# Performance work log

Measured on AMD Instinct MI355X. Metric: run time of the kernel, lower is better.

## Reference

```python
import jax, jax.numpy as jnp
import numpy as np

N_NODES = 50000
N_EDGES = 640000
IN_F, HID, OUT = 128, 128, 64
EPS = 1e-5


def _glorot(key, shape):
    fan_in, fan_out = shape
    lim = jnp.sqrt(6.0 / (fan_in + fan_out))
    return jax.random.uniform(key, shape, jnp.float32, -lim, lim)


def setup_inputs() -> dict:
    key = jax.random.key(0)
    ks = jax.random.split(key, 16)
    inp = {
        "x": jax.random.normal(ks[0], (N_NODES, IN_F), jnp.float32),
        "src": jax.random.randint(ks[1], (N_EDGES,), 0, N_NODES, jnp.int32),
        "dst": jax.random.randint(ks[2], (N_EDGES,), 0, N_NODES, jnp.int32),
        # layer 0: in -> hid
        "Ws0": _glorot(ks[3], (IN_F, HID)),
        "Wn0": _glorot(ks[4], (IN_F, HID)),
        "b0": jnp.zeros((HID,), jnp.float32),
        # layer 1: hid -> hid
        "Ws1": _glorot(ks[5], (HID, HID)),
        "Wn1": _glorot(ks[6], (HID, HID)),
        "b1": jnp.zeros((HID,), jnp.float32),
        # layer 2: hid -> out
        "Ws2": _glorot(ks[7], (HID, OUT)),
        "Wn2": _glorot(ks[8], (HID, OUT)),
        "b2": jnp.zeros((OUT,), jnp.float32),
        # batchnorm params for the two hidden layers
        "g0": jnp.ones((HID,), jnp.float32),
        "beta0": jnp.zeros((HID,), jnp.float32),
        "g1": jnp.ones((HID,), jnp.float32),
        "beta1": jnp.zeros((HID,), jnp.float32),
    }
    return inp


def _sage_conv(h, src, dst, Ws, Wn, b):
    # mean aggregation over in-neighbors (DGL SAGEConv 'mean')
    ones = jnp.ones_like(dst, dtype=h.dtype)
    deg = jax.ops.segment_sum(ones, dst, num_segments=N_NODES)
    agg = jax.ops.segment_sum(h[src], dst, num_segments=N_NODES)
    agg = agg / jnp.maximum(deg, 1.0)[:, None]
    return h @ Ws + agg @ Wn + b


def _batchnorm(h, gamma, beta):
    mu = jnp.mean(h, axis=0)
    var = jnp.mean(jnp.square(h - mu), axis=0)  # biased, like torch BN
    return (h - mu) * jax.lax.rsqrt(var + EPS) * gamma + beta


def reference(x, src, dst, Ws0, Wn0, b0, Ws1, Wn1, b1, Ws2, Wn2, b2,
              g0, beta0, g1, beta1):
    h = _sage_conv(x, src, dst, Ws0, Wn0, b0)
    h = jax.nn.relu(_batchnorm(h, g0, beta0))  # dropout = identity (eval)
    h = _sage_conv(h, src, dst, Ws1, Wn1, b1)
    h = jax.nn.relu(_batchnorm(h, g1, beta1))
    h = _sage_conv(h, src, dst, Ws2, Wn2, b2)
    return h
```

## Files before the change

### kernel.cpp

```cpp
#include <hip/hip_runtime.h>

#define N_NODES 50000
#define N_EDGES 640000
#define EPS 1e-5f
#define NBLK_SCAN 196

typedef __attribute__((ext_vector_type(8))) short short8;
typedef __attribute__((ext_vector_type(4))) float f32x4;

__device__ inline unsigned short f2bf(float f) {
    unsigned u = __float_as_uint(f);
    u += 0x7fffu + ((u >> 16) & 1u);
    return (unsigned short)(u >> 16);
}
__device__ inline float bf2f(unsigned short b) {
    return __uint_as_float(((unsigned)b) << 16);
}
__device__ inline void storev(short* p, float v) { *(unsigned short*)p = f2bf(v); }
__device__ inline void storev(float* p, float v) { *p = v; }

__global__ void hist_kernel(const int* __restrict__ dst, int* __restrict__ counts,
                            int* __restrict__ erank) {
    int i = blockIdx.x * 256 + threadIdx.x;
    if (i >= N_EDGES / 8) return;
    int4 a = ((const int4*)dst)[2 * i];
    int4 b = ((const int4*)dst)[2 * i + 1];
    int4 ra, rb;
    ra.x = atomicAdd(&counts[a.x], 1);
    ra.y = atomicAdd(&counts[a.y], 1);
    ra.z = atomicAdd(&counts[a.z], 1);
    ra.w = atomicAdd(&counts[a.w], 1);
    rb.x = atomicAdd(&counts[b.x], 1);
    rb.y = atomicAdd(&counts[b.y], 1);
    rb.z = atomicAdd(&counts[b.z], 1);
    rb.w = atomicAdd(&counts[b.w], 1);
    ((int4*)erank)[2 * i]     = ra;
    ((int4*)erank)[2 * i + 1] = rb;
}

__global__ void scan1_kernel(const int* __restrict__ counts, int* __restrict__ incl,
                             int* __restrict__ bsums) {
    __shared__ int tmp[256];
    int t = threadIdx.x;
    int i = blockIdx.x * 256 + t;
    tmp[t] = (i < N_NODES) ? counts[i] : 0;
    __syncthreads();
    for (int off = 1; off < 256; off <<= 1) {
        int add = (t >= off) ? tmp[t - off] : 0;
        __syncthreads();
        tmp[t] += add;
        __syncthreads();
    }
    if (i < N_NODES) incl[i] = tmp[t];
    if (t == 255) bsums[blockIdx.x] = tmp[255];
}

__global__ void scan2_kernel(const int* __restrict__ bsums, int* __restrict__ boff) {
    __shared__ int tmp[256];
    int t = threadIdx.x;
    tmp[t] = (t < NBLK_SCAN) ? bsums[t] : 0;
    __syncthreads();
    for (int off = 1; off < 256; off <<= 1) {
        int add = (t >= off) ? tmp[t - off] : 0;
        __syncthreads();
        tmp[t] += add;
        __syncthreads();
    }
    if (t < NBLK_SCAN) boff[t] = (t == 0) ? 0 : tmp[t - 1];
}

__global__ void scan3_kernel(const int* __restrict__ counts, const int* __restrict__ incl,
                             const int* __restrict__ boff, int* __restrict__ rowptr,
                             float* __restrict__ rdeg) {
    int i = blockIdx.x * 256 + threadIdx.x;
    if (i >= N_NODES) return;
    int c = counts[i];
    int inc = incl[i] + boff[blockIdx.x];
    rowptr[i] = inc - c;
    rdeg[i] = 1.0f / fmaxf((float)c, 1.0f);
    if (i == N_NODES - 1) rowptr[N_NODES] = inc;
}

__global__ void fill_kernel(const int* __restrict__ src, const int* __restrict__ dst,
                            const int* __restrict__ erank, const int* __restrict__ rowptr,
                            int* __restrict__ esrc) {
    int i = blockIdx.x * 256 + threadIdx.x;
    if (i >= N_EDGES / 8) return;
    int4 da = ((const int4*)dst)[2 * i];
    int4 db = ((const int4*)dst)[2 * i + 1];
    int4 sa = ((const int4*)src)[2 * i];
    int4 sb = ((const int4*)src)[2 * i + 1];
    int4 ra = ((const int4*)erank)[2 * i];
    int4 rb = ((const int4*)erank)[2 * i + 1];
    esrc[rowptr[da.x] + ra.x] = sa.x;
    esrc[rowptr[da.y] + ra.y] = sa.y;
    esrc[rowptr[da.z] + ra.z] = sa.z;
    esrc[rowptr[da.w] + ra.w] = sa.w;
    esrc[rowptr[db.x] + rb.x] = sb.x;
    esrc[rowptr[db.y] + rb.y] = sb.y;
    esrc[rowptr[db.z] + rb.z] = sb.z;
    esrc[rowptr[db.w] + rb.w] = sb.w;
}

__global__ void xcvt_kernel(const float* __restrict__ in, short* __restrict__ outp,
                            int* __restrict__ counts, float* __restrict__ stats) {
    int bi = blockIdx.x, t = threadIdx.x;
    if (bi == 0 && t < 128) {
        float4 z = make_float4(0.f, 0.f, 0.f, 0.f);
        ((float4*)stats)[t] = z;
    }
    if (bi >= 1 && bi <= NBLK_SCAN) {
        int idx = (bi - 1) * 256 + t;
        if (idx < N_NODES) counts[idx] = 0;
    }
    int i = bi * 256 + t;
    if (i >= N_NODES * 16) return;
    const float4* p = (const float4*)in + 2 * (size_t)i;
    float4 a = p[0], b = p[1];
    short8 v;
    v[0] = (short)f2bf(a.x); v[1] = (short)f2bf(a.y);
    v[2] = (short)f2bf(a.z); v[3] = (short)f2bf(a.w);
    v[4] = (short)f2bf(b.x); v[5] = (short)f2bf(b.y);
    v[6] = (short)f2bf(b.z); v[7] = (short)f2bf(b.w);
    *((short8*)outp + i) = v;
}

__global__ void pack_all(const float* __restrict__ W0, const float* __restrict__ W1,
                         const float* __restrict__ W2, const float* __restrict__ W3,
                         const float* __restrict__ W4, const float* __restrict__ W5,
                         short* __restrict__ P0, short* __restrict__ P1,
                         short* __restrict__ P2, short* __restrict__ P3,
                         short* __restrict__ P4, short* __restrict__ P5) {
    int b = blockIdx.x;
    const float* W; short* P; int NC; int base;
    if      (b < 8)  { W = W0; P = P0; NC = 128; base = 0;  }
    else if (b < 16) { W = W1; P = P1; NC = 128; base = 8;  }
    else if (b < 24) { W = W2; P = P2; NC = 128; base = 16; }
    else if (b < 32) { W = W3; P = P3; NC = 128; base = 24; }
    else if (b < 36) { W = W4; P = P4; NC = 64;  base = 32; }
    else             { W = W5; P = P5; NC = 64;  base = 36; }
    int idx = (b - base) * 256 + threadIdx.x;
    int total = 4 * (NC / 16) * 64;
    if (idx >= total) return;
    int lane = idx & 63;
    int cbks = idx >> 6;
    int cb = cbks % (NC / 16);
    int ks = cbks / (NC / 16);
    int col = cb * 16 + (lane & 15);
    int k0 = ks * 32 + ((lane >> 4) << 3);
    short8 v;
    #pragma unroll
    for (int j = 0; j < 8; ++j) v[j] = (short)f2bf(W[(size_t)(k0 + j) * NC + col]);
    *((short8*)P + idx) = v;
}

template<bool BN>
__global__ void gather_k(const short* __restrict__ h, const int* __restrict__ rowptr,
                         const int* __restrict__ esrc, const float* __restrict__ rdeg,
                         const float* __restrict__ sums, const float* __restrict__ sqs,
                         const float* __restrict__ g, const float* __restrict__ beta,
                         short* __restrict__ agg) {
    int node = blockIdx.x * 4 + (threadIdx.x >> 6);
    int lane = threadIdx.x & 63;
    if (node >= N_NODES) return;
    int beg = rowptr[node], end = rowptr[node + 1];
    float s0 = 0.f, s1 = 0.f, b0 = 0.f, b1 = 0.f;
    if (BN) {
        const float invN = 1.0f / N_NODES;
        float2 sm = *(const float2*)(sums + lane * 2);
        float2 sq = *(const float2*)(sqs + lane * 2);
        float2 gg = *(const float2*)(g + lane * 2);
        float2 bb = *(const float2*)(beta + lane * 2);
        float m0 = sm.x * invN, m1 = sm.y * invN;
        float v0 = sq.x * invN - m0 * m0, v1 = sq.y * invN - m1 * m1;
        s0 = rsqrtf(v0 + EPS) * gg.x;
        s1 = rsqrtf(v1 + EPS) * gg.y;
        b0 = bb.x - m0 * s0;
        b1 = bb.y - m1 * s1;
    }
    float ax = 0.f, ay = 0.f;
    while (beg < end) {
        int cnt = min(end - beg, 64);
        int mi = esrc[beg + min(lane, cnt - 1)];
        for (int j = 0; j < cnt; j += 16) {
            int lim = cnt - j; if (lim > 16) lim = 16;
            unsigned v[16];
            #pragma unroll
            for (int u = 0; u < 16; ++u) {
                int s = __shfl(mi, j + (u < lim ? u : lim - 1));
                v[u] = *(const unsigned*)(h + (size_t)s * 128 + lane * 2);
            }
            #pragma unroll
            for (int u = 0; u < 16; ++u) {
                if (u < lim) {
                    float lo = __uint_as_float(v[u] << 16);
                    float hi = __uint_as_float(v[u] & 0xffff0000u);
                    if (BN) {
                        lo = fmaxf(fmaf(lo, s0, b0), 0.f);
                        hi = fmaxf(fmaf(hi, s1, b1), 0.f);
                    }
                    ax += lo; ay += hi;
                }
            }
        }
        beg += cnt;
    }
    float r = rdeg[node];
    unsigned o = ((unsigned)f2bf(ay * r) << 16) | (unsigned)f2bf(ax * r);
    *(unsigned*)(agg + (size_t)node * 128 + lane * 2) = o;
}

template<int NC, bool BNIN, bool STATS, typename OUT>
__global__ __launch_bounds__(512, 4)
void sage_mfma(const short* __restrict__ h, const short* __restrict__ agg,
               const short* __restrict__ Wpk,
               const float* __restrict__ bias,
               const float* __restrict__ sums_in, const float* __restrict__ sqs_in,
               const float* __restrict__ g_in, const float* __restrict__ beta_in,
               float* __restrict__ sums, float* __restrict__ sqs,
               OUT* __restrict__ out) {
    constexpr int CBF = NC / 16;
    constexpr int WSH8 = CBF * 256;
    __shared__ short8 wlds[2 * WSH8];
    __shared__ float ls[128], lq[128];
    const int t = threadIdx.x;
    const int lane = t & 63;
    const int w = t >> 6;
    const int wrow = blockIdx.x * 128 + w * 16;
    const int arow = wrow + (lane & 15);
    const int koff = (lane >> 4) << 3;

    {
        const short8* gw = (const short8*)Wpk;
        #pragma unroll
        for (int i = 0; i < (2 * WSH8) / 512; ++i)
            wlds[t + i * 512] = gw[t + i * 512];
    }
    if (BNIN) {
        if (t < 128) {
            const float invN = 1.0f / N_NODES;
            float m = sums_in[t] * invN;
            float v = sqs_in[t] * invN - m * m;
            float sc = rsqrtf(v + EPS) * g_in[t];
            ls[t] = sc;
            lq[t] = beta_in[t] - m * sc;
        }
    }
    __syncthreads();

    short8 zero8 = {0, 0, 0, 0, 0, 0, 0, 0};
    short8 A[8];
    if (arow < N_NODES) {
        const short8* hb = (const short8*)(h + (size_t)arow * 128 + koff);
        const short8* ab = (const short8*)(agg + (size_t)arow * 128 + koff);
        #pragma unroll
        for (int ks = 0; ks < 4; ++ks) {
            A[ks] = hb[ks * 4];
            A[4 + ks] = ab[ks * 4];
        }
        if (BNIN) {
            #pragma unroll
            for (int ks = 0; ks < 4; ++ks) {
                int base = ks * 32 + koff;
                float4 sc0 = *(const float4*)&ls[base];
                float4 sc1 = *(const float4*)&ls[base + 4];
                float4 sh0 = *(const float4*)&lq[base];
                float4 sh1 = *(const float4*)&lq[base + 4];
                float scv[8] = {sc0.x, sc0.y, sc0.z, sc0.w, sc1.x, sc1.y, sc1.z, sc1.w};
                float shv[8] = {sh0.x, sh0.y, sh0.z, sh0.w, sh1.x, sh1.y, sh1.z, sh1.w};
                short8 v = A[ks];
                #pragma unroll
                for (int j = 0; j < 8; ++j) {
                    float f = bf2f((unsigned short)v[j]);
                    f = fmaxf(fmaf(f, scv[j], shv[j]), 0.f);
                    v[j] = (short)f2bf(f);
                }
                A[ks] = v;
            }
        }
    } else {
        #pragma unroll
        for (int s = 0; s < 8; ++s) A[s] = zero8;
    }

    if (STATS) {
        if (BNIN) __syncthreads();
        if (t < NC) { ls[t] = 0.f; lq[t] = 0.f; }
        __syncthreads();
    }

    f32x4 zacc = {0.f, 0.f, 0.f, 0.f};
    f32x4 acc[CBF];
    #pragma unroll
    for (int c = 0; c < CBF; ++c) acc[c] = zacc;

    #pragma unroll
    for (int s = 0; s < 8; ++s) {
        const int base = (s < 4) ? s * CBF * 64 : WSH8 + (s - 4) * CBF * 64;
        short8 af = A[s];
        #pragma unroll
        for (int c = 0; c < CBF; ++c) {
            short8 b = wlds[base + c * 64 + lane];
            acc[c] = __builtin_amdgcn_mfma_f32_16x16x32_bf16(af, b, acc[c], 0, 0, 0);
        }
    }

    const int col16 = lane & 15;
    const int rbase = wrow + ((lane >> 4) << 2);
    #pragma unroll
    for (int c = 0; c < CBF; ++c) {
        int gcol = c * 16 + col16;
        float bb = bias[gcol];
        float ps = 0.f, pq = 0.f;
        #pragma unroll
        for (int r = 0; r < 4; ++r) {
            int row = rbase + r;
            if (row < N_NODES) {
                float val = acc[c][r] + bb;
                storev(out + (size_t)row * NC + gcol, val);
                if (STATS) { ps += val; pq += val * val; }
            }
        }
        if (STATS) {
            ps += __shfl_xor(ps, 16); ps += __shfl_xor(ps, 32);
            pq += __shfl_xor(pq, 16); pq += __shfl_xor(pq, 32);
            if (lane < 16) {
                atomicAdd(&ls[gcol], ps);
                atomicAdd(&lq[gcol], pq);
            }
        }
    }
    if (STATS) {
        __syncthreads();
        if (t < NC) {
            atomicAdd(&sums[t], ls[t]);
            atomicAdd(&sqs[t], lq[t]);
        }
    }
}

extern "C" void kernel_launch(void* const* d_in, const int* in_sizes, int n_in,
                              void* d_out, int out_size, void* d_ws, size_t ws_size,
                              hipStream_t stream) {
    const float* x   = (const float*)d_in[0];
    const int*   src = (const int*)d_in[1];
    const int*   dst = (const int*)d_in[2];
    const float* Ws0 = (const float*)d_in[3];
    const float* Wn0 = (const float*)d_in[4];
    const float* b0  = (const float*)d_in[5];
    const float* Ws1 = (const float*)d_in[6];
    const float* Wn1 = (const float*)d_in[7];
    const float* b1  = (const float*)d_in[8];
    const float* Ws2 = (const float*)d_in[9];
    const float* Wn2 = (const float*)d_in[10];
    const float* b2  = (const float*)d_in[11];
    const float* g0  = (const float*)d_in[12];
    const float* bt0 = (const float*)d_in[13];
    const float* g1  = (const float*)d_in[14];
    const float* bt1 = (const float*)d_in[15];

    char* ws = (char*)d_ws;
    const size_t HB2 = (size_t)N_NODES * 128 * 2;
    size_t off = 0;
    short* xb     = (short*)(ws + off); off += HB2;
    short* aggb   = (short*)(ws + off); off += HB2;
    short* h1b    = (short*)(ws + off); off += HB2;
    short* h2b    = (short*)(ws + off); off += HB2;
    int*   esrc   = (int*)(ws + off);   off += (size_t)N_EDGES * 4;
    int*   erank  = (int*)(ws + off);   off += (size_t)N_EDGES * 4;
    int*   counts = (int*)(ws + off);   off += 200192;
    int*   incl   = (int*)(ws + off);   off += 200192;
    int*   rowptr = (int*)(ws + off);   off += 200704;
    float* rdeg   = (float*)(ws + off); off += 200192;
    int*   bsums  = (int*)(ws + off);   off += 1024;
    int*   boff   = (int*)(ws + off);   off += 1024;
    float* stats  = (float*)(ws + off); off += 2048;
    float* sums0  = stats;
    float* sqs0   = stats + 128;
    float* sums1  = stats + 256;
    float* sqs1   = stats + 384;
    short* pW0    = (short*)(ws + off); off += 65536;
    short* pW1    = (short*)(ws + off); off += 65536;
    short* pW2    = (short*)(ws + off); off += 32768;

    float* out = (float*)d_out;

    const int e8grid = (N_EDGES / 8 + 255) / 256;
    const int ggrid  = (N_NODES + 3) / 4;
    const int mgrid  = (N_NODES + 127) / 128;
    const int cgrid  = (N_NODES * 16 + 255) / 256;

    xcvt_kernel<<<cgrid, 256, 0, stream>>>(x, xb, counts, stats);
    pack_all<<<40, 256, 0, stream>>>(Ws0, Wn0, Ws1, Wn1, Ws2, Wn2,
                                     pW0, pW0 + 16384, pW1, pW1 + 16384,
                                     pW2, pW2 + 8192);
    hist_kernel<<<e8grid, 256, 0, stream>>>(dst, counts, erank);
    scan1_kernel<<<NBLK_SCAN, 256, 0, stream>>>(counts, incl, bsums);
    scan2_kernel<<<1, 256, 0, stream>>>(bsums, boff);
    scan3_kernel<<<NBLK_SCAN, 256, 0, stream>>>(counts, incl, boff, rowptr, rdeg);
    fill_kernel<<<e8grid, 256, 0, stream>>>(src, dst, erank, rowptr, esrc);

    gather_k<false><<<ggrid, 256, 0, stream>>>(xb, rowptr, esrc, rdeg,
                                               nullptr, nullptr, nullptr, nullptr, aggb);
    sage_mfma<128, false, true, short><<<mgrid, 512, 0, stream>>>(
        xb, aggb, pW0, b0, nullptr, nullptr, nullptr, nullptr, sums0, sqs0, h1b);

    gather_k<true><<<ggrid, 256, 0, stream>>>(h1b, rowptr, esrc, rdeg,
                                              sums0, sqs0, g0, bt0, aggb);
    sage_mfma<128, true, true, short><<<mgrid, 512, 0, stream>>>(
        h1b, aggb, pW1, b1, sums0, sqs0, g0, bt0, sums1, sqs1, h2b);

    gather_k<true><<<ggrid, 256, 0, stream>>>(h2b, rowptr, esrc, rdeg,
                                              sums1, sqs1, g1, bt1, aggb);
    sage_mfma<64, true, false, float><<<mgrid, 512, 0, stream>>>(
        h2b, aggb, pW2, b2, sums1, sqs1, g1, bt1, nullptr, nullptr, out);
}
```

Before: 203.5 us.

## Fuse neighbor mean-aggregation gather into the per-layer MFMA SAGE kernel

Removes the separate gather kernel and has each wave of the MFMA kernel first aggregate its own 16 rows' neighbors, applying the folded BatchNorm+ReLU from LDS. Results are written to the agg buffer and read back after a block barrier. This saves three kernel launches and keeps the agg traffic local to a block. In exchange, each wave walks 16 nodes one after another, and the grid shrinks to a few hundred 512-thread blocks, which may leave too little parallelism to hide gather latency.

Result: slower. 237.0 us (+16.5%).

```diff
diff --git a/kernel.cpp b/kernel.cpp
--- a/kernel.cpp
+++ b/kernel.cpp
@@ -154,71 +154,16 @@
     *((short8*)P + idx) = v;
 }
 
-template<bool BN>
-__global__ void gather_k(const short* __restrict__ h, const int* __restrict__ rowptr,
-                         const int* __restrict__ esrc, const float* __restrict__ rdeg,
-                         const float* __restrict__ sums, const float* __restrict__ sqs,
-                         const float* __restrict__ g, const float* __restrict__ beta,
-                         short* __restrict__ agg) {
-    int node = blockIdx.x * 4 + (threadIdx.x >> 6);
-    int lane = threadIdx.x & 63;
-    if (node >= N_NODES) return;
-    int beg = rowptr[node], end = rowptr[node + 1];
-    float s0 = 0.f, s1 = 0.f, b0 = 0.f, b1 = 0.f;
-    if (BN) {
-        const float invN = 1.0f / N_NODES;
-        float2 sm = *(const float2*)(sums + lane * 2);
-        float2 sq = *(const float2*)(sqs + lane * 2);
-        float2 gg = *(const float2*)(g + lane * 2);
-        float2 bb = *(const float2*)(beta + lane * 2);
-        float m0 = sm.x * invN, m1 = sm.y * invN;
-        float v0 = sq.x * invN - m0 * m0, v1 = sq.y * invN - m1 * m1;
-        s0 = rsqrtf(v0 + EPS) * gg.x;
-        s1 = rsqrtf(v1 + EPS) * gg.y;
-        b0 = bb.x - m0 * s0;
-        b1 = bb.y - m1 * s1;
-    }
-    float ax = 0.f, ay = 0.f;
-    while (beg < end) {
-        int cnt = min(end - beg, 64);
-        int mi = esrc[beg + min(lane, cnt - 1)];
-        for (int j = 0; j < cnt; j += 16) {
-            int lim = cnt - j; if (lim > 16) lim = 16;
-            unsigned v[16];
-            #pragma unroll
-            for (int u = 0; u < 16; ++u) {
-                int s = __shfl(mi, j + (u < lim ? u : lim - 1));
-                v[u] = *(const unsigned*)(h + (size_t)s * 128 + lane * 2);
-            }
-            #pragma unroll
-            for (int u = 0; u < 16; ++u) {
-                if (u < lim) {
-                    float lo = __uint_as_float(v[u] << 16);
-                    float hi = __uint_as_float(v[u] & 0xffff0000u);
-                    if (BN) {
-                        lo = fmaxf(fmaf(lo, s0, b0), 0.f);
-                        hi = fmaxf(fmaf(hi, s1, b1), 0.f);
-                    }
-                    ax += lo; ay += hi;
-                }
-            }
-        }
-        beg += cnt;
-    }
-    float r = rdeg[node];
-    unsigned o = ((unsigned)f2bf(ay * r) << 16) | (unsigned)f2bf(ax * r);
-    *(unsigned*)(agg + (size_t)node * 128 + lane * 2) = o;
-}
-
 template<int NC, bool BNIN, bool STATS, typename OUT>
 __global__ __launch_bounds__(512, 4)
-void sage_mfma(const short* __restrict__ h, const short* __restrict__ agg,
-               const short* __restrict__ Wpk,
-               const float* __restrict__ bias,
-               const float* __restrict__ sums_in, const float* __restrict__ sqs_in,
-               const float* __restrict__ g_in, const float* __restrict__ beta_in,
-               float* __restrict__ sums, float* __restrict__ sqs,
-               OUT* __restrict__ out) {
+void sage_fused(const short* __restrict__ h,
+                const int* __restrict__ rowptr, const int* __restrict__ esrc,
+                const float* __restrict__ rdeg,
+                const short* __restrict__ Wpk, const float* __restrict__ bias,
+                const float* __restrict__ sums_in, const float* __restrict__ sqs_in,
+                const float* __restrict__ g_in, const float* __restrict__ beta_in,
+                float* __restrict__ sums, float* __restrict__ sqs,
+                short* __restrict__ aggb, OUT* __restrict__ out) {
     constexpr int CBF = NC / 16;
     constexpr int WSH8 = CBF * 256;
     __shared__ short8 wlds[2 * WSH8];
@@ -248,11 +193,55 @@
     }
     __syncthreads();
 
+    {
+        float s0 = 0.f, s1 = 0.f, b0 = 0.f, b1 = 0.f;
+        if (BNIN) {
+            s0 = ls[lane * 2];     s1 = ls[lane * 2 + 1];
+            b0 = lq[lane * 2];     b1 = lq[lane * 2 + 1];
+        }
+        for (int n = 0; n < 16; ++n) {
+            int node = wrow + n;
+            if (node >= N_NODES) break;
+            int beg = rowptr[node], end = rowptr[node + 1];
+            float ax = 0.f, ay = 0.f;
+            while (beg < end) {
+                int cnt = min(end - beg, 64);
+                int mi = esrc[beg + min(lane, cnt - 1)];
+                for (int j = 0; j < cnt; j += 16) {
+                    int lim = cnt - j; if (lim > 16) lim = 16;
+                    unsigned v[16];
+                    #pragma unroll
+                    for (int u = 0; u < 16; ++u) {
+                        int s = __shfl(mi, j + (u < lim ? u : lim - 1));
+                        v[u] = *(const unsigned*)(h + (size_t)s * 128 + lane * 2);
+                    }
+                    #pragma unroll
+                    for (int u = 0; u < 16; ++u) {
+                        if (u < lim) {
+                            float lo = __uint_as_float(v[u] << 16);
+                            float hi = __uint_as_float(v[u] & 0xffff0000u);
+                            if (BNIN) {
+                                lo = fmaxf(fmaf(lo, s0, b0), 0.f);
+                                hi = fmaxf(fmaf(hi, s1, b1), 0.f);
+                            }
+                            ax += lo; ay += hi;
+                        }
+                    }
+                }
+                beg += cnt;
+            }
+            float r = rdeg[node];
+            unsigned o = ((unsigned)f2bf(ay * r) << 16) | (unsigned)f2bf(ax * r);
+            *(unsigned*)(aggb + (size_t)node * 128 + lane * 2) = o;
+        }
+    }
+    __syncthreads();
+
     short8 zero8 = {0, 0, 0, 0, 0, 0, 0, 0};
     short8 A[8];
     if (arow < N_NODES) {
         const short8* hb = (const short8*)(h + (size_t)arow * 128 + koff);
-        const short8* ab = (const short8*)(agg + (size_t)arow * 128 + koff);
+        const short8* ab = (const short8*)(aggb + (size_t)arow * 128 + koff);
         #pragma unroll
         for (int ks = 0; ks < 4; ++ks) {
             A[ks] = hb[ks * 4];
@@ -386,7 +375,6 @@
     float* out = (float*)d_out;
 
     const int e8grid = (N_EDGES / 8 + 255) / 256;
-    const int ggrid  = (N_NODES + 3) / 4;
     const int mgrid  = (N_NODES + 127) / 128;
     const int cgrid  = (N_NODES * 16 + 255) / 256;
 
@@ -400,18 +388,15 @@
     scan3_kernel<<<NBLK_SCAN, 256, 0, stream>>>(counts, incl, boff, rowptr, rdeg);
     fill_kernel<<<e8grid, 256, 0, stream>>>(src, dst, erank, rowptr, esrc);
 
-    gather_k<false><<<ggrid, 256, 0, stream>>>(xb, rowptr, esrc, rdeg,
-                                               nullptr, nullptr, nullptr, nullptr, aggb);
-    sage_mfma<128, false, true, short><<<mgrid, 512, 0, stream>>>(
-        xb, aggb, pW0, b0, nullptr, nullptr, nullptr, nullptr, sums0, sqs0, h1b);
-
-    gather_k<true><<<ggrid, 256, 0, stream>>>(h1b, rowptr, esrc, rdeg,
-                                              sums0, sqs0, g0, bt0, aggb);
-    sage_mfma<128, true, true, short><<<mgrid, 512, 0, stream>>>(
-        h1b, aggb, pW1, b1, sums0, sqs0, g0, bt0, sums1, sqs1, h2b);
-
-    gather_k<true><<<ggrid, 256, 0, stream>>>(h2b, rowptr, esrc, rdeg,
-                                              sums1, sqs1, g1, bt1, aggb);
-    sage_mfma<64, true, false, float><<<mgrid, 512, 0, stream>>>(
-        h2b, aggb, pW2, b2, sums1, sqs1, g1, bt1, nullptr, nullptr, out);
-}
+    sage_fused<128, false, true, short><<<mgrid, 512, 0, stream>>>(
+        xb, rowptr, esrc, rdeg, pW0, b0,
+        nullptr, nullptr, nullptr, nullptr, sums0, sqs0, aggb, h1b);
+
+    sage_fused<128, true, true, short><<<mgrid, 512, 0, stream>>>(
+        h1b, rowptr, esrc, rdeg, pW1, b1,
+        sums0, sqs0, g0, bt0, sums1, sqs1, aggb, h2b);
+
+    sage_fused<64, true, false, float><<<mgrid, 512, 0, stream>>>(
+        h2b, rowptr, esrc, rdeg, pW2, b2,
+        sums1, sqs1, g1, bt1, nullptr, nullptr, aggb, out);
+}
```

## Reorder last SAGE layer to transform-then-aggregate and fuse prep kernels

Applied to the files above, without the earlier changes.

For the final layer, the code now multiplies BN+ReLU-normalized features by Wn2 first, producing a 64-wide bf16 intermediate. It then gathers and averages that narrower tensor and adds it into the output, instead of gathering 128-wide features and multiplying afterward. This roughly halves the gather traffic for the last layer, at the cost of an extra bf16 rounding of the projected features and a read-modify-write of the output. The input conversion and weight packing kernels are also merged into one launch to save launch overhead.

New measurement: 193.5 us (median of 2 runs). 4.9% less time.

```diff
diff --git a/kernel.cpp b/kernel.cpp
--- a/kernel.cpp
+++ b/kernel.cpp
@@ -4,6 +4,7 @@
 #define N_EDGES 640000
 #define EPS 1e-5f
 #define NBLK_SCAN 196
+#define CGRID 3125
 
 typedef __attribute__((ext_vector_type(8))) short short8;
 typedef __attribute__((ext_vector_type(4))) float f32x4;
@@ -102,36 +103,37 @@
     esrc[rowptr[db.w] + rb.w] = sb.w;
 }
 
-__global__ void xcvt_kernel(const float* __restrict__ in, short* __restrict__ outp,
-                            int* __restrict__ counts, float* __restrict__ stats) {
+__global__ void prep_kernel(const float* __restrict__ in, short* __restrict__ outp,
+                            int* __restrict__ counts, float* __restrict__ stats,
+                            const float* __restrict__ W0, const float* __restrict__ W1,
+                            const float* __restrict__ W2, const float* __restrict__ W3,
+                            const float* __restrict__ W4, const float* __restrict__ W5,
+                            short* __restrict__ P0, short* __restrict__ P1,
+                            short* __restrict__ P2, short* __restrict__ P3,
+                            short* __restrict__ P4, short* __restrict__ P5) {
     int bi = blockIdx.x, t = threadIdx.x;
-    if (bi == 0 && t < 128) {
-        float4 z = make_float4(0.f, 0.f, 0.f, 0.f);
-        ((float4*)stats)[t] = z;
-    }
-    if (bi >= 1 && bi <= NBLK_SCAN) {
-        int idx = (bi - 1) * 256 + t;
-        if (idx < N_NODES) counts[idx] = 0;
-    }
-    int i = bi * 256 + t;
-    if (i >= N_NODES * 16) return;
-    const float4* p = (const float4*)in + 2 * (size_t)i;
-    float4 a = p[0], b = p[1];
-    short8 v;
-    v[0] = (short)f2bf(a.x); v[1] = (short)f2bf(a.y);
-    v[2] = (short)f2bf(a.z); v[3] = (short)f2bf(a.w);
-    v[4] = (short)f2bf(b.x); v[5] = (short)f2bf(b.y);
-    v[6] = (short)f2bf(b.z); v[7] = (short)f2bf(b.w);
-    *((short8*)outp + i) = v;
-}
-
-__global__ void pack_all(const float* __restrict__ W0, const float* __restrict__ W1,
-                         const float* __restrict__ W2, const float* __restrict__ W3,
-                         const float* __restrict__ W4, const float* __restrict__ W5,
-                         short* __restrict__ P0, short* __restrict__ P1,
-                         short* __restrict__ P2, short* __restrict__ P3,
-                         short* __restrict__ P4, short* __restrict__ P5) {
-    int b = blockIdx.x;
+    if (bi < CGRID) {
+        if (bi == 0 && t < 128) {
+            float4 z = make_float4(0.f, 0.f, 0.f, 0.f);
+            ((float4*)stats)[t] = z;
+        }
+        if (bi >= 1 && bi <= NBLK_SCAN) {
+            int idx = (bi - 1) * 256 + t;
+            if (idx < N_NODES) counts[idx] = 0;
+        }
+        int i = bi * 256 + t;
+        if (i >= N_NODES * 16) return;
+        const float4* p = (const float4*)in + 2 * (size_t)i;
+        float4 a = p[0], b = p[1];
+        short8 v;
+        v[0] = (short)f2bf(a.x); v[1] = (short)f2bf(a.y);
+        v[2] = (short)f2bf(a.z); v[3] = (short)f2bf(a.w);
+        v[4] = (short)f2bf(b.x); v[5] = (short)f2bf(b.y);
+        v[6] = (short)f2bf(b.z); v[7] = (short)f2bf(b.w);
+        *((short8*)outp + i) = v;
+        return;
+    }
+    int b = bi - CGRID;
     const float* W; short* P; int NC; int base;
     if      (b < 8)  { W = W0; P = P0; NC = 128; base = 0;  }
     else if (b < 16) { W = W1; P = P1; NC = 128; base = 8;  }
@@ -139,7 +141,7 @@
     else if (b < 32) { W = W3; P = P3; NC = 128; base = 24; }
     else if (b < 36) { W = W4; P = P4; NC = 64;  base = 32; }
     else             { W = W5; P = P5; NC = 64;  base = 36; }
-    int idx = (b - base) * 256 + threadIdx.x;
+    int idx = (b - base) * 256 + t;
     int total = 4 * (NC / 16) * 64;
     if (idx >= total) return;
     int lane = idx & 63;
@@ -339,6 +341,147 @@
     }
 }
 
+__global__ __launch_bounds__(512, 4)
+void sage_mfma2(const short* __restrict__ h, const short* __restrict__ Wpk,
+                const float* __restrict__ bias,
+                const float* __restrict__ sums_in, const float* __restrict__ sqs_in,
+                const float* __restrict__ g_in, const float* __restrict__ beta_in,
+                float* __restrict__ out, short* __restrict__ z2) {
+    constexpr int CBF = 4;
+    constexpr int WSH8 = 1024;
+    __shared__ short8 wlds[2 * WSH8];
+    __shared__ float ls[128], lq[128];
+    const int t = threadIdx.x;
+    const int lane = t & 63;
+    const int w = t >> 6;
+    const int wrow = blockIdx.x * 128 + w * 16;
+    const int arow = wrow + (lane & 15);
+    const int koff = (lane >> 4) << 3;
+
+    {
+        const short8* gw = (const short8*)Wpk;
+        #pragma unroll
+        for (int i = 0; i < (2 * WSH8) / 512; ++i)
+            wlds[t + i * 512] = gw[t + i * 512];
+    }
+    if (t < 128) {
+        const float invN = 1.0f / N_NODES;
+        float m = sums_in[t] * invN;
+        float v = sqs_in[t] * invN - m * m;
+        float sc = rsqrtf(v + EPS) * g_in[t];
+        ls[t] = sc;
+        lq[t] = beta_in[t] - m * sc;
+    }
+    __syncthreads();
+
+    short8 zero8 = {0, 0, 0, 0, 0, 0, 0, 0};
+    short8 A[4];
+    if (arow < N_NODES) {
+        const short8* hb = (const short8*)(h + (size_t)arow * 128 + koff);
+        #pragma unroll
+        for (int ks = 0; ks < 4; ++ks) {
+            int base = ks * 32 + koff;
+            float4 sc0 = *(const float4*)&ls[base];
+            float4 sc1 = *(const float4*)&ls[base + 4];
+            float4 sh0 = *(const float4*)&lq[base];
+            float4 sh1 = *(const float4*)&lq[base + 4];
+            float scv[8] = {sc0.x, sc0.y, sc0.z, sc0.w, sc1.x, sc1.y, sc1.z, sc1.w};
+            float shv[8] = {sh0.x, sh0.y, sh0.z, sh0.w, sh1.x, sh1.y, sh1.z, sh1.w};
+            short8 v = hb[ks * 4];
+            #pragma unroll
+            for (int j = 0; j < 8; ++j) {
+                float f = bf2f((unsigned short)v[j]);
+                f = fmaxf(fmaf(f, scv[j], shv[j]), 0.f);
+                v[j] = (short)f2bf(f);
+            }
+            A[ks] = v;
+        }
+    } else {
+        #pragma unroll
+        for (int s = 0; s < 4; ++s) A[s] = zero8;
+    }
+
+    f32x4 zacc = {0.f, 0.f, 0.f, 0.f};
+    f32x4 accy[CBF], accz[CBF];
+    #pragma unroll
+    for (int c = 0; c < CBF; ++c) { accy[c] = zacc; accz[c] = zacc; }
+
+    #pragma unroll
+    for (int s = 0; s < 4; ++s) {
+        short8 af = A[s];
+        #pragma unroll
+        for (int c = 0; c < CBF; ++c) {
+            short8 by = wlds[s * 256 + c * 64 + lane];
+            accy[c] = __builtin_amdgcn_mfma_f32_16x16x32_bf16(af, by, accy[c], 0, 0, 0);
+        }
+        #pragma unroll
+        for (int c = 0; c < CBF; ++c) {
+            short8 bz = wlds[WSH8 + s * 256 + c * 64 + lane];
+            accz[c] = __builtin_amdgcn_mfma_f32_16x16x32_bf16(af, bz, accz[c], 0, 0, 0);
+        }
+    }
+
+    const int col16 = lane & 15;
+    const int rbase = wrow + ((lane >> 4) << 2);
+    #pragma unroll
+    for (int c = 0; c < CBF; ++c) {
+        int gcol = c * 16 + col16;
+        float bb = bias[gcol];
+        #pragma unroll
+        for (int r = 0; r < 4; ++r) {
+            int row = rbase + r;
+            if (row < N_NODES) {
+                out[(size_t)row * 64 + gcol] = accy[c][r] + bb;
+                storev(z2 + (size_t)row * 64 + gcol, accz[c][r]);
+            }
+        }
+    }
+}
+
+__global__ void gather64_add(const short* __restrict__ z2, const int* __restrict__ rowptr,
+                             const int* __restrict__ esrc, const float* __restrict__ rdeg,
+                             float* __restrict__ out) {
+    int node = blockIdx.x * 4 + (threadIdx.x >> 6);
+    int lane = threadIdx.x & 63;
+    if (node >= N_NODES) return;
+    const int e = lane >> 5;
+    const int p = lane & 31;
+    int beg = rowptr[node], end = rowptr[node + 1];
+    float a0 = 0.f, a1 = 0.f;
+    while (beg < end) {
+        int cnt = min(end - beg, 64);
+        int mi = esrc[beg + min(lane, cnt - 1)];
+        for (int j = 0; j < cnt; j += 16) {
+            unsigned v[8];
+            #pragma unroll
+            for (int u = 0; u < 8; ++u) {
+                int idx = j + 2 * u + e;
+                int s = __shfl(mi, min(idx, cnt - 1));
+                v[u] = *(const unsigned*)(z2 + (size_t)s * 64 + p * 2);
+            }
+            #pragma unroll
+            for (int u = 0; u < 8; ++u) {
+                int idx = j + 2 * u + e;
+                if (idx < cnt) {
+                    a0 += __uint_as_float(v[u] << 16);
+                    a1 += __uint_as_float(v[u] & 0xffff0000u);
+                }
+            }
+        }
+        beg += cnt;
+    }
+    a0 += __shfl_xor(a0, 32);
+    a1 += __shfl_xor(a1, 32);
+    if (e == 0) {
+        float r = rdeg[node];
+        float2* po = (float2*)(out + (size_t)node * 64 + p * 2);
+        float2 y = *po;
+        y.x += a0 * r;
+        y.y += a1 * r;
+        *po = y;
+    }
+}
+
 extern "C" void kernel_launch(void* const* d_in, const int* in_sizes, int n_in,
                               void* d_out, int out_size, void* d_ws, size_t ws_size,
                               hipStream_t stream) {
@@ -366,6 +509,7 @@
     short* aggb   = (short*)(ws + off); off += HB2;
     short* h1b    = (short*)(ws + off); off += HB2;
     short* h2b    = (short*)(ws + off); off += HB2;
+    short* z2b    = (short*)(ws + off); off += (size_t)N_NODES * 64 * 2;
     int*   esrc   = (int*)(ws + off);   off += (size_t)N_EDGES * 4;
     int*   erank  = (int*)(ws + off);   off += (size_t)N_EDGES * 4;
     int*   counts = (int*)(ws + off);   off += 200192;
@@ -388,12 +532,10 @@
     const int e8grid = (N_EDGES / 8 + 255) / 256;
     const int ggrid  = (N_NODES + 3) / 4;
     const int mgrid  = (N_NODES + 127) / 128;
-    const int cgrid  = (N_NODES * 16 + 255) / 256;
-
-    xcvt_kernel<<<cgrid, 256, 0, stream>>>(x, xb, counts, stats);
-    pack_all<<<40, 256, 0, stream>>>(Ws0, Wn0, Ws1, Wn1, Ws2, Wn2,
-                                     pW0, pW0 + 16384, pW1, pW1 + 16384,
-                                     pW2, pW2 + 8192);
+
+    prep_kernel<<<CGRID + 40, 256, 0, stream>>>(
+        x, xb, counts, stats, Ws0, Wn0, Ws1, Wn1, Ws2, Wn2,
+        pW0, pW0 + 16384, pW1, pW1 + 16384, pW2, pW2 + 8192);
     hist_kernel<<<e8grid, 256, 0, stream>>>(dst, counts, erank);
     scan1_kernel<<<NBLK_SCAN, 256, 0, stream>>>(counts, incl, bsums);
     scan2_kernel<<<1, 256, 0, stream>>>(bsums, boff);
@@ -410,8 +552,7 @@
     sage_mfma<128, true, true, short><<<mgrid, 512, 0, stream>>>(
         h1b, aggb, pW1, b1, sums0, sqs0, g0, bt0, sums1, sqs1, h2b);
 
-    gather_k<true><<<ggrid, 256, 0, stream>>>(h2b, rowptr, esrc, rdeg,
-                                              sums1, sqs1, g1, bt1, aggb);
-    sage_mfma<64, true, false, float><<<mgrid, 512, 0, stream>>>(
-        h2b, aggb, pW2, b2, sums1, sqs1, g1, bt1, nullptr, nullptr, out);
-}
+    sage_mfma2<<<mgrid, 512, 0, stream>>>(
+        h2b, pW2, b2, sums1, sqs1, g1, bt1, out, z2b);
+    gather64_add<<<ggrid, 256, 0, stream>>>(z2b, rowptr, esrc, rdeg, out);
+}
```
